# Performance work log

Measured on AMD Instinct MI355X. Metric: run time of the kernel, lower is better.

Reference implementation:

```python
import jax, jax.numpy as jnp
import numpy as np

N_NODES, N_RELS, D, DEG = 100000, 2000, 128, 16
N_EDGES = N_NODES * DEG


def setup_inputs() -> dict:
    key = jax.random.key(0)
    k1, k2, k3, k4, k5 = jax.random.split(key, 5)
    # subject column: sorted and covers every node (tf.math.segment_sum requires
    # sorted segment ids; full coverage avoids 0/0 in the normalization)
    subj = jnp.repeat(jnp.arange(N_NODES, dtype=jnp.int64), DEG)
    rel = jax.random.randint(k1, (N_EDGES,), 0, N_RELS, dtype=jnp.int64)
    obj = jax.random.randint(k2, (N_EDGES,), 0, N_NODES, dtype=jnp.int64)
    triples = jnp.stack([subj, rel, obj], axis=1)[None]  # [1, E, 3]
    features = jax.random.normal(k3, (N_NODES, D), jnp.float32)
    rel_emb = jax.random.normal(k4, (N_RELS, D), jnp.float32)
    attn_kernel = jax.random.normal(k5, (D, 1), jnp.float32) * 0.05  # keep exp() finite
    return {"triples": triples, "features": features, "rel_emb": rel_emb,
            "attn_kernel": attn_kernel}


def reference(triples, features, rel_emb, attn_kernel):
    # single head, 'concat' reduction, linear activation, no bias
    t = jnp.squeeze(triples, 0).astype(jnp.int32)  # [E, 3]
    subj, rel_idx, obj_idx = t[:, 0], t[:, 1], t[:, 2]
    n = features.shape[0]

    obj_embs = features[obj_idx]          # [E, D] gather
    edge_embs = rel_emb[rel_idx]          # [E, D] gather

    # tf.nn.l2_normalize(edge_embs, 1) with eps 1e-12
    edge_n = edge_embs * jax.lax.rsqrt(
        jnp.maximum(jnp.sum(edge_embs * edge_embs, axis=1, keepdims=True), 1e-12))
    # Householder-like reflection (note: projection onto normalized dir, scaled
    # by the UNnormalized edge embedding, exactly as in the source)
    refl = jnp.sum(obj_embs * edge_n, axis=1, keepdims=True) * edge_embs
    obj_embs = obj_embs - 2.0 * refl      # [E, D]

    # per-relation attention logit, gathered per edge
    att_value = jnp.exp(rel_emb @ attn_kernel)[rel_idx]  # [E, 1]

    num = jax.ops.segment_sum(att_value * obj_embs, subj, num_segments=n)  # [N, D]
    den = jax.ops.segment_sum(att_value, subj, num_segments=n)             # [N, 1]
    return num / den
```

## Files before the change

### kernel.cpp

```cpp
#include <hip/hip_runtime.h>
#include <hip/hip_fp16.h>

#define N_NODES 100000
#define N_RELS  2000
#define D       128
#define DEG     16

#define RELWS_BYTES  16384
#define FEAT16_BYTES ((size_t)N_NODES * D * 2)
#define REL16_BYTES  ((size_t)N_RELS * D * 2)
#define WS_NEED      (RELWS_BYTES + FEAT16_BYTES + REL16_BYTES)

typedef unsigned int u32x4 __attribute__((ext_vector_type(4)));

static __device__ __forceinline__ __half2 bc_h2(unsigned int u) {
  return __builtin_bit_cast(__half2, u);
}
static __device__ __forceinline__ int bc_i(float f) {
  return __builtin_bit_cast(int, f);
}
static __device__ __forceinline__ float bc_f(int i) {
  return __builtin_bit_cast(float, i);
}

static __device__ __forceinline__ float row16_sum_bcast(float v) {
  v += bc_f(__builtin_amdgcn_update_dpp(0, bc_i(v), 0x0B1, 0xF, 0xF, false));
  v += bc_f(__builtin_amdgcn_update_dpp(0, bc_i(v), 0x04E, 0xF, 0xF, false));
  v += bc_f(__builtin_amdgcn_update_dpp(0, bc_i(v), 0x124, 0xF, 0xF, false));
  v += bc_f(__builtin_amdgcn_update_dpp(0, bc_i(v), 0x128, 0xF, 0xF, false));
  return v;
}

__global__ __launch_bounds__(256) void pre_kernel(
    const float* __restrict__ features,
    const float* __restrict__ rel_emb,
    const float* __restrict__ attn,
    float2* __restrict__ relws,
    unsigned int* __restrict__ rel16u,
    uint2* __restrict__ feat16v) {
  const int i = blockIdx.x * 256 + threadIdx.x;
  float4 v = ((const float4*)features)[i];
  uint2 o;
  o.x = __builtin_bit_cast(unsigned int, __builtin_amdgcn_cvt_pkrtz(v.x, v.y));
  o.y = __builtin_bit_cast(unsigned int, __builtin_amdgcn_cvt_pkrtz(v.z, v.w));
  feat16v[i] = o;

  if (blockIdx.x < N_RELS / 4) {
    const int wave = threadIdx.x >> 6;
    const int lane = threadIdx.x & 63;
    const int r = blockIdx.x * 4 + wave;
    float2 ev = *(const float2*)(rel_emb + (size_t)r * D + lane * 2);
    float2 av = *(const float2*)(attn + lane * 2);
    rel16u[r * 64 + lane] =
        __builtin_bit_cast(unsigned int, __builtin_amdgcn_cvt_pkrtz(ev.x, ev.y));
    float ss = ev.x * ev.x + ev.y * ev.y;
    float dt = ev.x * av.x + ev.y * av.y;
#pragma unroll
    for (int off = 32; off >= 1; off >>= 1) {
      ss += __shfl_xor(ss, off, 64);
      dt += __shfl_xor(dt, off, 64);
    }
    if (lane == 0) {
      float inv = rsqrtf(fmaxf(ss, 1e-12f));
      relws[r] = make_float2(inv, expf(dt));
    }
  }
}

__global__ __launch_bounds__(256) void rel_pre_kernel(
    const float* __restrict__ rel_emb,
    const float* __restrict__ attn,
    float2* __restrict__ relws,
    unsigned int* __restrict__ rel16u) {
  const int wave = threadIdx.x >> 6;
  const int lane = threadIdx.x & 63;
  const int r = blockIdx.x * 4 + wave;
  float2 ev = *(const float2*)(rel_emb + (size_t)r * D + lane * 2);
  float2 av = *(const float2*)(attn + lane * 2);
  rel16u[r * 64 + lane] =
      __builtin_bit_cast(unsigned int, __builtin_amdgcn_cvt_pkrtz(ev.x, ev.y));
  float ss = ev.x * ev.x + ev.y * ev.y;
  float dt = ev.x * av.x + ev.y * av.y;
#pragma unroll
  for (int off = 32; off >= 1; off >>= 1) {
    ss += __shfl_xor(ss, off, 64);
    dt += __shfl_xor(dt, off, 64);
  }
  if (lane == 0) {
    float inv = rsqrtf(fmaxf(ss, 1e-12f));
    relws[r] = make_float2(inv, expf(dt));
  }
}


#define GAT_WAIT(n) asm volatile("s_waitcnt vmcnt(" #n ")")

#define GAT_STAGE(ofv, efv, rx)                                                \
  {                                                                            \
    const unsigned long long fo_ =                                             \
        (unsigned long long)(feat16 + (size_t)((rx) >> 11) * D + s * 8);       \
    const unsigned long long fe_ =                                             \
        (unsigned long long)(rel16 + (size_t)((rx) & 2047u) * D + s * 8);      \
    asm volatile("global_load_dwordx4 %0, %1, off" : "=v"(ofv) : "v"(fo_));    \
    asm volatile("global_load_dwordx4 %0, %1, off" : "=v"(efv) : "v"(fe_));    \
  }

#define GAT_BODY(of, ef, ac)                                                   \
  {                                                                            \
    const __half2 o0 = bc_h2((of).x), o1 = bc_h2((of).y),                      \
                  o2 = bc_h2((of).z), o3 = bc_h2((of).w);                      \
    const __half2 e0 = bc_h2((ef).x), e1 = bc_h2((ef).y),                      \
                  e2 = bc_h2((ef).z), e3 = bc_h2((ef).w);                      \
    __half2 pp = __hmul2(o0, e0);                                              \
    pp = __hfma2(o1, e1, pp);                                                  \
    pp = __hfma2(o2, e2, pp);                                                  \
    pp = __hfma2(o3, e3, pp);                                                  \
    const float pd = row16_sum_bcast(__low2float(pp) + __high2float(pp));      \
    const __half2 h = bc_h2(ac);                                               \
    const __half2 att2 = __half2half2(__low2half(h));                          \
    const __half2 c2 = __float2half2_rn(__high2float(h) * pd);                 \
    acc1_0 = __hfma2(att2, o0, acc1_0);                                        \
    acc1_1 = __hfma2(att2, o1, acc1_1);                                        \
    acc1_2 = __hfma2(att2, o2, acc1_2);                                        \
    acc1_3 = __hfma2(att2, o3, acc1_3);                                        \
    acc2_0 = __hfma2(c2, e0, acc2_0);                                          \
    acc2_1 = __hfma2(c2, e1, acc2_1);                                          \
    acc2_2 = __hfma2(c2, e2, acc2_2);                                          \
    acc2_3 = __hfma2(c2, e3, acc2_3);                                          \
  }

#define GAT_FULL(i, j, vmw)                                                    \
  GAT_WAIT(vmw);                                                               \
  __builtin_amdgcn_sched_barrier(0);                                           \
  GAT_STAGE(of##j, ef##j, rc##j.x);                                            \
  GAT_BODY(of##i, ef##i, rc##i.y)

#define GAT_LAST(i, vmw)                                                       \
  GAT_WAIT(vmw);                                                               \
  __builtin_amdgcn_sched_barrier(0);                                           \
  GAT_BODY(of##i, ef##i, rc##i.y)

__global__ __launch_bounds__(256, 3) void gat16_kernel(
    const int* __restrict__ triples,
    const unsigned short* __restrict__ feat16,
    const unsigned short* __restrict__ rel16,
    const float2* __restrict__ relws,
    float* __restrict__ out) {
  __shared__ uint2 recs[256];

  const int tid  = threadIdx.x;
  const int s    = tid & 15;
  const int g    = (tid >> 4) & 3;
  const int wave = tid >> 6;
  const int node = blockIdx.x * 16 + wave * 4 + g;

  const int* t = triples + (size_t)node * (DEG * 3);
  const int tr = t[3 * s + 1];
  const int to = t[3 * s + 2];
  const float2 ia = relws[tr];
  const float att = ia.y;
  const float cf  = 2.f * att * ia.x;

  float den = att;
  den += __shfl_xor(den, 1);
  den += __shfl_xor(den, 2);
  den += __shfl_xor(den, 4);
  den += __shfl_xor(den, 8);
  const float rden = 1.f / den;

  recs[tid] = make_uint2(
      (unsigned int)((to << 11) | tr),
      __builtin_bit_cast(unsigned int, __builtin_amdgcn_cvt_pkrtz(att, cf)));
  __syncthreads();

  const int rbase = tid & 0xF0;

  const uint2 rc0  = recs[rbase + 0],  rc1  = recs[rbase + 1];
  const uint2 rc2  = recs[rbase + 2],  rc3  = recs[rbase + 3];
  const uint2 rc4  = recs[rbase + 4],  rc5  = recs[rbase + 5];
  const uint2 rc6  = recs[rbase + 6],  rc7  = recs[rbase + 7];
  const uint2 rc8  = recs[rbase + 8],  rc9  = recs[rbase + 9];
  const uint2 rc10 = recs[rbase + 10], rc11 = recs[rbase + 11];
  const uint2 rc12 = recs[rbase + 12], rc13 = recs[rbase + 13];
  const uint2 rc14 = recs[rbase + 14], rc15 = recs[rbase + 15];

  u32x4 of0, of1, of2, of3, of4, of5, of6, of7;
  u32x4 of8, of9, of10, of11, of12, of13, of14, of15;
  u32x4 ef0, ef1, ef2, ef3, ef4, ef5, ef6, ef7;
  u32x4 ef8, ef9, ef10, ef11, ef12, ef13, ef14, ef15;

  GAT_WAIT(0);
  GAT_STAGE(of0, ef0, rc0.x);
  GAT_STAGE(of1, ef1, rc1.x);
  GAT_STAGE(of2, ef2, rc2.x);
  GAT_STAGE(of3, ef3, rc3.x);
  GAT_STAGE(of4, ef4, rc4.x);
  GAT_STAGE(of5, ef5, rc5.x);
  GAT_STAGE(of6, ef6, rc6.x);
  GAT_STAGE(of7, ef7, rc7.x);

  __half2 acc1_0 = __float2half2_rn(0.f), acc1_1 = __float2half2_rn(0.f);
  __half2 acc1_2 = __float2half2_rn(0.f), acc1_3 = __float2half2_rn(0.f);
  __half2 acc2_0 = __float2half2_rn(0.f), acc2_1 = __float2half2_rn(0.f);
  __half2 acc2_2 = __float2half2_rn(0.f), acc2_3 = __float2half2_rn(0.f);

  GAT_FULL(0, 8, 14);
  GAT_FULL(1, 9, 14);
  GAT_FULL(2, 10, 14);
  GAT_FULL(3, 11, 14);
  GAT_FULL(4, 12, 14);
  GAT_FULL(5, 13, 14);
  GAT_FULL(6, 14, 14);
  GAT_FULL(7, 15, 14);
  GAT_LAST(8, 14);
  GAT_LAST(9, 12);
  GAT_LAST(10, 10);
  GAT_LAST(11, 8);
  GAT_LAST(12, 6);
  GAT_LAST(13, 4);
  GAT_LAST(14, 2);
  GAT_LAST(15, 0);

  float* op = out + (size_t)node * D + s * 8;
  float4 r0, r1;
  {
    float2 a0 = __half22float2(acc1_0), b0 = __half22float2(acc2_0);
    float2 a1 = __half22float2(acc1_1), b1 = __half22float2(acc2_1);
    r0.x = (a0.x - b0.x) * rden; r0.y = (a0.y - b0.y) * rden;
    r0.z = (a1.x - b1.x) * rden; r0.w = (a1.y - b1.y) * rden;
    float2 a2 = __half22float2(acc1_2), b2 = __half22float2(acc2_2);
    float2 a3 = __half22float2(acc1_3), b3 = __half22float2(acc2_3);
    r1.x = (a2.x - b2.x) * rden; r1.y = (a2.y - b2.y) * rden;
    r1.z = (a3.x - b3.x) * rden; r1.w = (a3.y - b3.y) * rden;
  }
  *(float4*)op = r0;
  *(float4*)(op + 4) = r1;
}

__global__ __launch_bounds__(256) void gat_kernel(
    const int* __restrict__ triples,
    const float* __restrict__ features,
    const float* __restrict__ rel_emb,
    const float2* __restrict__ relws,
    float* __restrict__ out) {
  const int wave = threadIdx.x >> 6;
  const int lane = threadIdx.x & 63;
  const int node = blockIdx.x * 4 + wave;
  const int* t = triples + (size_t)node * DEG * 3;
  int tv = (lane < DEG * 3) ? t[lane] : 0;
  float2 acc = make_float2(0.f, 0.f);
  float den = 0.f;
#pragma unroll
  for (int i = 0; i < DEG; ++i) {
    const int rel = __builtin_amdgcn_readfirstlane(__shfl(tv, 3 * i + 1, 64));
    const int obj = __builtin_amdgcn_readfirstlane(__shfl(tv, 3 * i + 2, 64));
    float2 ia = relws[rel];
    float2 ov = *(const float2*)(features + (size_t)obj * D + lane * 2);
    float2 ev = *(const float2*)(rel_emb + (size_t)rel * D + lane * 2);
    float pd = ov.x * ev.x + ov.y * ev.y;
#pragma unroll
    for (int off = 32; off >= 1; off >>= 1) pd += __shfl_xor(pd, off, 64);
    const float c = 2.f * pd * ia.x;
    const float att = ia.y;
    acc.x += att * (ov.x - c * ev.x);
    acc.y += att * (ov.y - c * ev.y);
    den += att;
  }
  const float r = 1.f / den;
  *(float2*)(out + (size_t)node * D + lane * 2) =
      make_float2(acc.x * r, acc.y * r);
}

extern "C" void kernel_launch(void* const* d_in, const int* in_sizes, int n_in,
                              void* d_out, int out_size, void* d_ws, size_t ws_size,
                              hipStream_t stream) {
  const int*   triples  = (const int*)d_in[0];
  const float* features = (const float*)d_in[1];
  const float* rel_emb  = (const float*)d_in[2];
  const float* attn     = (const float*)d_in[3];
  float*       out      = (float*)d_out;

  float2* relws = (float2*)d_ws;

  if (ws_size >= WS_NEED) {
    unsigned short* feat16 = (unsigned short*)((char*)d_ws + RELWS_BYTES);
    unsigned int*   rel16u = (unsigned int*)((char*)d_ws + RELWS_BYTES + FEAT16_BYTES);
    pre_kernel<<<(N_NODES * D / 4) / 256, 256, 0, stream>>>(
        features, rel_emb, attn, relws, rel16u, (uint2*)feat16);
    gat16_kernel<<<N_NODES / 16, 256, 0, stream>>>(
        triples, feat16, (const unsigned short*)rel16u, relws, out);
  } else {
    rel_pre_kernel<<<N_RELS / 4, 256, 0, stream>>>(rel_emb, attn, relws,
                                                   (unsigned int*)d_ws);
    gat_kernel<<<N_NODES / 4, 256, 0, stream>>>(
        triples, features, rel_emb, relws, out);
  }
}
```

Baseline: 169.5 us.

## Stage edge gathers through LDS ring via direct global-to-LDS DMA loads

Replaces register-resident prefetch of 16 feature/relation gathers per edge with a 6-slot per-wave LDS ring filled by global_load_lds (direct-to-LDS) loads, then read back with ds_read_b128. This frees the many VGPRs held by in-flight gathers, allowing higher occupancy (launch bound min-blocks removed). It adds an LDS round-trip and lgkmcnt waits per edge, and reduces prefetch depth from 8 to 6 edges in flight per wave.

```diff
diff --git a/kernel.cpp b/kernel.cpp
--- a/kernel.cpp
+++ b/kernel.cpp
@@ -5,6 +5,7 @@
 #define N_RELS  2000
 #define D       128
 #define DEG     16
+#define PIPE    6
 
 #define RELWS_BYTES  16384
 #define FEAT16_BYTES ((size_t)N_NODES * D * 2)
@@ -21,6 +22,12 @@
 }
 static __device__ __forceinline__ float bc_f(int i) {
   return __builtin_bit_cast(float, i);
+}
+
+static __device__ __forceinline__ void ldsdma16(const void* g, void* l) {
+  __builtin_amdgcn_global_load_lds(
+      (const __attribute__((address_space(1))) unsigned int*)g,
+      (__attribute__((address_space(3))) unsigned int*)l, 16, 0, 0);
 }
 
 static __device__ __forceinline__ float row16_sum_bcast(float v) {
@@ -93,16 +100,16 @@
 }
 
 
-#define GAT_WAIT(n) asm volatile("s_waitcnt vmcnt(" #n ")")
-
-#define GAT_STAGE(ofv, efv, rx)                                                \
+#define GAT_WAITV(n) asm volatile("s_waitcnt vmcnt(" #n ")" ::: "memory")
+#define GAT_WAITL()  asm volatile("s_waitcnt lgkmcnt(0)" ::: "memory")
+#define GAT_SB()     __builtin_amdgcn_sched_barrier(0)
+
+#define GAT_STAGE(slot, rx)                                                    \
   {                                                                            \
-    const unsigned long long fo_ =                                             \
-        (unsigned long long)(feat16 + (size_t)((rx) >> 11) * D + s * 8);       \
-    const unsigned long long fe_ =                                             \
-        (unsigned long long)(rel16 + (size_t)((rx) & 2047u) * D + s * 8);      \
-    asm volatile("global_load_dwordx4 %0, %1, off" : "=v"(ofv) : "v"(fo_));    \
-    asm volatile("global_load_dwordx4 %0, %1, off" : "=v"(efv) : "v"(fe_));    \
+    ldsdma16(feat16 + (size_t)((rx) >> 11) * D + s * 8,                        \
+             (void*)&ring[wave][(slot)][0]);                                   \
+    ldsdma16(rel16 + (size_t)((rx) & 2047u) * D + s * 8,                       \
+             (void*)&ring[wave][(slot)][64]);                                  \
   }
 
 #define GAT_BODY(of, ef, ac)                                                   \
@@ -129,24 +136,42 @@
     acc2_3 = __hfma2(c2, e3, acc2_3);                                          \
   }
 
-#define GAT_FULL(i, j, vmw)                                                    \
-  GAT_WAIT(vmw);                                                               \
-  __builtin_amdgcn_sched_barrier(0);                                           \
-  GAT_STAGE(of##j, ef##j, rc##j.x);                                            \
-  GAT_BODY(of##i, ef##i, rc##i.y)
-
-#define GAT_LAST(i, vmw)                                                       \
-  GAT_WAIT(vmw);                                                               \
-  __builtin_amdgcn_sched_barrier(0);                                           \
-  GAT_BODY(of##i, ef##i, rc##i.y)
-
-__global__ __launch_bounds__(256, 3) void gat16_kernel(
+#define GAT_CONS_S(slot, vmw, rcur, rnext)                                     \
+  {                                                                            \
+    GAT_WAITV(vmw);                                                            \
+    GAT_SB();                                                                  \
+    u32x4 of_, ef_;                                                            \
+    const unsigned fa_ = rb + (slot) * 2048;                                   \
+    asm volatile("ds_read_b128 %0, %1" : "=v"(of_) : "v"(fa_));                \
+    asm volatile("ds_read_b128 %0, %1 offset:1024" : "=v"(ef_) : "v"(fa_));    \
+    GAT_WAITL();                                                               \
+    GAT_SB();                                                                  \
+    GAT_STAGE((slot), rnext.x);                                                \
+    GAT_SB();                                                                  \
+    GAT_BODY(of_, ef_, rcur.y);                                                \
+  }
+
+#define GAT_CONS_D(slot, vmw, rcur)                                            \
+  {                                                                            \
+    GAT_WAITV(vmw);                                                            \
+    GAT_SB();                                                                  \
+    u32x4 of_, ef_;                                                            \
+    const unsigned fa_ = rb + (slot) * 2048;                                   \
+    asm volatile("ds_read_b128 %0, %1" : "=v"(of_) : "v"(fa_));                \
+    asm volatile("ds_read_b128 %0, %1 offset:1024" : "=v"(ef_) : "v"(fa_));    \
+    GAT_WAITL();                                                               \
+    GAT_SB();                                                                  \
+    GAT_BODY(of_, ef_, rcur.y);                                                \
+  }
+
+__global__ __launch_bounds__(256) void gat16_kernel(
     const int* __restrict__ triples,
     const unsigned short* __restrict__ feat16,
     const unsigned short* __restrict__ rel16,
     const float2* __restrict__ relws,
     float* __restrict__ out) {
   __shared__ uint2 recs[256];
+  __shared__ uint4 ring[4][PIPE][128];
 
   const int tid  = threadIdx.x;
   const int s    = tid & 15;
@@ -184,42 +209,38 @@
   const uint2 rc12 = recs[rbase + 12], rc13 = recs[rbase + 13];
   const uint2 rc14 = recs[rbase + 14], rc15 = recs[rbase + 15];
 
-  u32x4 of0, of1, of2, of3, of4, of5, of6, of7;
-  u32x4 of8, of9, of10, of11, of12, of13, of14, of15;
-  u32x4 ef0, ef1, ef2, ef3, ef4, ef5, ef6, ef7;
-  u32x4 ef8, ef9, ef10, ef11, ef12, ef13, ef14, ef15;
-
-  GAT_WAIT(0);
-  GAT_STAGE(of0, ef0, rc0.x);
-  GAT_STAGE(of1, ef1, rc1.x);
-  GAT_STAGE(of2, ef2, rc2.x);
-  GAT_STAGE(of3, ef3, rc3.x);
-  GAT_STAGE(of4, ef4, rc4.x);
-  GAT_STAGE(of5, ef5, rc5.x);
-  GAT_STAGE(of6, ef6, rc6.x);
-  GAT_STAGE(of7, ef7, rc7.x);
+  const unsigned rb =
+      (unsigned)(unsigned long long)&ring[wave][0][0] + (tid & 63) * 16;
 
   __half2 acc1_0 = __float2half2_rn(0.f), acc1_1 = __float2half2_rn(0.f);
   __half2 acc1_2 = __float2half2_rn(0.f), acc1_3 = __float2half2_rn(0.f);
   __half2 acc2_0 = __float2half2_rn(0.f), acc2_1 = __float2half2_rn(0.f);
   __half2 acc2_2 = __float2half2_rn(0.f), acc2_3 = __float2half2_rn(0.f);
 
-  GAT_FULL(0, 8, 14);
-  GAT_FULL(1, 9, 14);
-  GAT_FULL(2, 10, 14);
-  GAT_FULL(3, 11, 14);
-  GAT_FULL(4, 12, 14);
-  GAT_FULL(5, 13, 14);
-  GAT_FULL(6, 14, 14);
-  GAT_FULL(7, 15, 14);
-  GAT_LAST(8, 14);
-  GAT_LAST(9, 12);
-  GAT_LAST(10, 10);
-  GAT_LAST(11, 8);
-  GAT_LAST(12, 6);
-  GAT_LAST(13, 4);
-  GAT_LAST(14, 2);
-  GAT_LAST(15, 0);
+  GAT_WAITV(0);
+  GAT_STAGE(0, rc0.x);
+  GAT_STAGE(1, rc1.x);
+  GAT_STAGE(2, rc2.x);
+  GAT_STAGE(3, rc3.x);
+  GAT_STAGE(4, rc4.x);
+  GAT_STAGE(5, rc5.x);
+
+  GAT_CONS_S(0, 10, rc0, rc6);
+  GAT_CONS_S(1, 10, rc1, rc7);
+  GAT_CONS_S(2, 10, rc2, rc8);
+  GAT_CONS_S(3, 10, rc3, rc9);
+  GAT_CONS_S(4, 10, rc4, rc10);
+  GAT_CONS_S(5, 10, rc5, rc11);
+  GAT_CONS_S(0, 10, rc6, rc12);
+  GAT_CONS_S(1, 10, rc7, rc13);
+  GAT_CONS_S(2, 10, rc8, rc14);
+  GAT_CONS_S(3, 10, rc9, rc15);
+  GAT_CONS_D(4, 10, rc10);
+  GAT_CONS_D(5, 8,  rc11);
+  GAT_CONS_D(0, 6,  rc12);
+  GAT_CONS_D(1, 4,  rc13);
+  GAT_CONS_D(2, 2,  rc14);
+  GAT_CONS_D(3, 0,  rc15);
 
   float* op = out + (size_t)node * D + s * 8;
   float4 r0, r1;
```

Result: no change. 168.1 us (-0.8%).
